# Kernel tuning notes

Measured on AMD Instinct MI355X. Metric: run time of the kernel, lower is better.

## Reference

```python
import jax, jax.numpy as jnp
import numpy as np

B, T, D = 1, 2048, 2048
H, HD = 32, 64
HEAD_COUNTS = np.array([8, 6, 4, 4, 6, 4])  # reasoning, creativity, curiosity, emotional, memory, meta
NEG = -1e9


def rope_tables(seq_len, dim, dtype):
    inv_freq = 1.0 / (10000.0 ** (jnp.arange(0, dim, 2, dtype=jnp.float32) / dim))
    t = jnp.arange(seq_len, dtype=jnp.float32)
    freqs = jnp.outer(t, inv_freq)            # [T, dim/2]
    emb = jnp.concatenate([freqs, freqs], -1) # [T, dim]
    return jnp.cos(emb).astype(dtype), jnp.sin(emb).astype(dtype)


def rotate_half(x):
    x1, x2 = jnp.split(x, 2, axis=-1)
    return jnp.concatenate([-x2, x1], axis=-1)


def setup_inputs() -> dict:
    key = jax.random.key(0)
    ks = jax.random.split(key, 8)
    x = jax.random.normal(ks[0], (B, T, D), jnp.float32)
    mask = jnp.tril(jnp.ones((T, T), jnp.int32))[None, None]  # causal [1,1,T,T]
    context_bias = jax.random.normal(ks[1], (B, T, T), jnp.float32) * 0.02
    mod_weights = jax.random.uniform(ks[2], (B, 6), jnp.float32, 0.5, 1.5)
    Wq = jax.random.normal(ks[3], (D, D), jnp.float32) * 0.02
    Wk = jax.random.normal(ks[4], (D, D), jnp.float32) * 0.02
    Wv = jax.random.normal(ks[5], (D, D), jnp.float32) * 0.02
    Wo = jax.random.normal(ks[6], (D, D), jnp.float32) * 0.02
    temp_scales = jnp.ones((H,), jnp.float32)
    return {"x": x, "mask": mask, "context_bias": context_bias,
            "mod_weights": mod_weights, "Wq": Wq, "Wk": Wk, "Wv": Wv,
            "Wo": Wo, "temp_scales": temp_scales}


def reference(x, mask, context_bias, mod_weights, Wq, Wk, Wv, Wo, temp_scales):
    b, t, d = x.shape
    # projections (torch Linear: y = x @ W.T)
    Q = (x @ Wq.T).reshape(b, t, H, HD).transpose(0, 2, 1, 3)  # [B,H,T,HD]
    K = (x @ Wk.T).reshape(b, t, H, HD).transpose(0, 2, 1, 3)
    V = (x @ Wv.T).reshape(b, t, H, HD).transpose(0, 2, 1, 3)
    cos, sin = rope_tables(t, HD, x.dtype)
    cos, sin = cos[None, None], sin[None, None]
    Q = Q * cos + rotate_half(Q) * sin
    K = K * cos + rotate_half(K) * sin
    scale = (HD ** -0.5) * temp_scales.reshape(1, H, 1, 1)
    attn = jnp.einsum('bhqd,bhkd->bhqk', Q, K) * scale
    attn = jnp.where(mask == 0, NEG, attn)
    attn = attn + context_bias[:, None]
    # per-head module reweight: expand [B,6] -> [B,H]
    w = jnp.repeat(mod_weights, np.asarray(HEAD_COUNTS), axis=1, total_repeat_length=H)
    attn = attn * w[:, :, None, None]
    attn = jax.nn.softmax(attn, axis=-1)
    out = jnp.einsum('bhqk,bhkd->bhqd', attn, V)
    out = out.transpose(0, 2, 1, 3).reshape(b, t, d)
    return out @ Wo.T
```

## Files before the change

kernel.cpp:

```cpp
#include <hip/hip_runtime.h>
#include <hip/hip_bf16.h>
#include <cstdint>
#include <cstddef>

typedef __bf16 bf16;
typedef bf16 bf16x4 __attribute__((ext_vector_type(4)));
typedef bf16 bf16x8 __attribute__((ext_vector_type(8)));
typedef float f32x4 __attribute__((ext_vector_type(4)));

#define MFMA_BF16(a,b,c) __builtin_amdgcn_mfma_f32_16x16x32_bf16((a),(b),(c),0,0,0)

typedef __attribute__((address_space(1))) const void gvoid;
typedef __attribute__((address_space(3))) void svoid;
__device__ __forceinline__ void gload16(const bf16* g, bf16* l){
  __builtin_amdgcn_global_load_lds((gvoid*)g, (svoid*)l, 16, 0, 0);
}

__device__ __forceinline__ int head_group(int h){
  return (h<8)?0:(h<14)?1:(h<18)?2:(h<22)?3:(h<28)?4:5;
}

struct CvtArgs { const float* src[5]; bf16* dst[5]; };
__global__ __launch_bounds__(256) void cvt_rope_kernel(CvtArgs a, int n,
                                                       float* __restrict__ cosT,
                                                       float* __restrict__ sinT){
  const int z = blockIdx.y;
  if (z == 5){
    if (blockIdx.x >= 256) return;
    const int t = blockIdx.x*8 + (threadIdx.x>>5);
    const int i = threadIdx.x&31;
    float invf = powf(10000.0f, -((float)i)/32.0f);
    float ang = (float)t * invf;
    cosT[t*32+i] = cosf(ang);
    sinT[t*32+i] = sinf(ang);
    return;
  }
  const float* __restrict__ in = a.src[z];
  bf16* __restrict__ out = a.dst[z];
  int i = (blockIdx.x*256 + threadIdx.x)*8;
  if (i >= n) return;
  const float4* p = (const float4*)(in + i);
  float4 va = p[0], vb = p[1];
  bf16x8 o;
  o[0]=(bf16)va.x; o[1]=(bf16)va.y; o[2]=(bf16)va.z; o[3]=(bf16)va.w;
  o[4]=(bf16)vb.x; o[5]=(bf16)vb.y; o[6]=(bf16)vb.z; o[7]=(bf16)vb.w;
  *(bf16x8*)(out+i) = o;
}

__device__ __forceinline__ void gemm_core(const bf16* __restrict__ A,
                                          const bf16* __restrict__ B,
                                          int row0, int col0,
                                          f32x4 (&acc)[4][4]){
  __shared__ bf16 As[128*32];
  __shared__ bf16 Bs[128*32];
  const int tid  = threadIdx.x;
  const int wave = tid>>6, lane = tid&63;
  const int l16  = lane&15, lg = lane>>4;
  const int wr   = wave>>1, wc = wave&1;

  const bf16* Ag0 = A + (size_t)(row0 + wave*32      + (lane>>2))*2048 + (lane&3)*8;
  const bf16* Ag1 = A + (size_t)(row0 + wave*32 + 16 + (lane>>2))*2048 + (lane&3)*8;
  const bf16* Bg0 = B + (size_t)(col0 + wave*32      + (lane>>2))*2048 + (lane&3)*8;
  const bf16* Bg1 = B + (size_t)(col0 + wave*32 + 16 + (lane>>2))*2048 + (lane&3)*8;
  bf16* AsB0 = As + (wave*32     )*32;
  bf16* AsB1 = As + (wave*32 + 16)*32;
  bf16* BsB0 = Bs + (wave*32     )*32;
  bf16* BsB1 = Bs + (wave*32 + 16)*32;

  #pragma unroll
  for (int m=0;m<4;++m)
    #pragma unroll
    for (int n=0;n<4;++n)
      #pragma unroll
      for (int r=0;r<4;++r) acc[m][n][r] = 0.f;

  for (int kt=0; kt<64; ++kt){
    const int ko = kt*32;
    gload16(Ag0 + ko, AsB0);
    gload16(Ag1 + ko, AsB1);
    gload16(Bg0 + ko, BsB0);
    gload16(Bg1 + ko, BsB1);
    __syncthreads();
    bf16x8 af[4], bfr[4];
    #pragma unroll
    for (int m=0;m<4;++m) af[m]  = *(const bf16x8*)&As[(wr*64+m*16+l16)*32 + lg*8];
    #pragma unroll
    for (int n=0;n<4;++n) bfr[n] = *(const bf16x8*)&Bs[(wc*64+n*16+l16)*32 + lg*8];
    #pragma unroll
    for (int m=0;m<4;++m)
      #pragma unroll
      for (int n=0;n<4;++n)
        acc[m][n] = MFMA_BF16(af[m], bfr[n], acc[m][n]);
    __syncthreads();
  }
}

__global__ __launch_bounds__(256) void gemm_qkv_kernel(
    const bf16* __restrict__ A,
    const bf16* __restrict__ B0, const bf16* __restrict__ B1, const bf16* __restrict__ B2,
    bf16* __restrict__ Qs, bf16* __restrict__ Ks, bf16* __restrict__ Vt,
    const float* __restrict__ cosT, const float* __restrict__ sinT,
    const float* __restrict__ mw, const float* __restrict__ ts){
  const int z = blockIdx.z;
  const bf16* B = (z==0)?B0:((z==1)?B1:B2);
  const int row0 = blockIdx.y*128, col0 = blockIdx.x*128;

  f32x4 acc[4][4];
  gemm_core(A, B, row0, col0, acc);

  const int tid  = threadIdx.x;
  const int wave = tid>>6, lane = tid&63;
  const int l16  = lane&15, lg = lane>>4;
  const int wr   = wave>>1, wc = wave&1;
  const int h    = (col0 + wc*64) >> 6;

  if (z == 2){
    #pragma unroll
    for (int n=0;n<4;++n){
      const int d = n*16 + l16;
      #pragma unroll
      for (int m=0;m<4;++m){
        const int t0 = row0 + wr*64 + m*16 + lg*4;
        bf16x4 v;
        #pragma unroll
        for (int r=0;r<4;++r) v[r] = (bf16)acc[m][n][r];
        *(bf16x4*)&Vt[((size_t)h*64 + d)*2048 + t0] = v;
      }
    }
  } else {
    const float sc = (z==0) ? 0.125f*ts[h]*mw[head_group(h)] : 1.0f;
    bf16* Out = (z==0) ? Qs : Ks;
    #pragma unroll
    for (int m=0;m<4;++m){
      #pragma unroll
      for (int r=0;r<4;++r){
        const int t = row0 + wr*64 + m*16 + lg*4 + r;
        const float* ct = cosT + t*32;
        const float* st = sinT + t*32;
        bf16* dst = Out + ((size_t)h*2048 + t)*64;
        #pragma unroll
        for (int n=0;n<2;++n){
          const int i = n*16 + l16;
          const float c = ct[i], s = st[i];
          const float a1 = acc[m][n][r], a2 = acc[m][n+2][r];
          dst[i]    = (bf16)((a1*c - a2*s)*sc);
          dst[i+32] = (bf16)((a2*c + a1*s)*sc);
        }
      }
    }
  }
}

__global__ __launch_bounds__(256) void gemm_out_kernel(
    const bf16* __restrict__ A, const bf16* __restrict__ B, float* __restrict__ C){
  __shared__ bf16 As[128*32];
  __shared__ bf16 Bs[64*32];
  const int row0 = blockIdx.y*128, col0 = blockIdx.x*64;
  const int tid  = threadIdx.x;
  const int wave = tid>>6, lane = tid&63;
  const int l16  = lane&15, lg = lane>>4;
  const int wr   = wave>>1, wc = wave&1;

  const bf16* Ag0 = A + (size_t)(row0 + wave*32      + (lane>>2))*2048 + (lane&3)*8;
  const bf16* Ag1 = A + (size_t)(row0 + wave*32 + 16 + (lane>>2))*2048 + (lane&3)*8;
  const bf16* Bg0 = B + (size_t)(col0 + wave*16      + (lane>>2))*2048 + (lane&3)*8;
  bf16* AsB0 = As + (wave*32     )*32;
  bf16* AsB1 = As + (wave*32 + 16)*32;
  bf16* BsB0 = Bs + (wave*16     )*32;

  f32x4 acc[4][2];
  #pragma unroll
  for (int m=0;m<4;++m)
    #pragma unroll
    for (int n=0;n<2;++n)
      #pragma unroll
      for (int r=0;r<4;++r) acc[m][n][r] = 0.f;

  for (int kt=0; kt<64; ++kt){
    const int ko = kt*32;
    gload16(Ag0 + ko, AsB0);
    gload16(Ag1 + ko, AsB1);
    gload16(Bg0 + ko, BsB0);
    __syncthreads();
    bf16x8 af[4], bfr[2];
    #pragma unroll
    for (int m=0;m<4;++m) af[m]  = *(const bf16x8*)&As[(wr*64+m*16+l16)*32 + lg*8];
    #pragma unroll
    for (int n=0;n<2;++n) bfr[n] = *(const bf16x8*)&Bs[(wc*32+n*16+l16)*32 + lg*8];
    #pragma unroll
    for (int m=0;m<4;++m)
      #pragma unroll
      for (int n=0;n<2;++n)
        acc[m][n] = MFMA_BF16(af[m], bfr[n], acc[m][n]);
    __syncthreads();
  }

  #pragma unroll
  for (int m=0;m<4;++m)
    #pragma unroll
    for (int n=0;n<2;++n)
      #pragma unroll
      for (int r=0;r<4;++r){
        size_t idx = (size_t)(row0 + wr*64 + m*16 + lg*4 + r)*2048
                   + col0 + wc*32 + n*16 + l16;
        C[idx] = acc[m][n][r];
      }
}

__global__ __launch_bounds__(512) void attn_kernel(
    const bf16* __restrict__ Qs, const bf16* __restrict__ Ks,
    const bf16* __restrict__ Vt, const float* __restrict__ biasf,
    const float* __restrict__ mw, bf16* __restrict__ attout){
  const int n  = blockIdx.x;
  const int h  = ((n&7)<<2) | ((n>>3)&3);
  const int qt = (n&256) ? ((n>>5)&7) : 15-((n>>5)&7);
  const int tid = threadIdx.x, wid = tid>>6, lane = tid&63;
  const int l16 = lane&15, lg = lane>>4;
  const float w_h = mw[head_group(h)];
  const int qbase = qt*128 + wid*16;
  const int qg0 = qbase + lg*4;
  const int nkt = 2*qt + 2;

  __shared__ bf16 Kl[2][4096];
  __shared__ bf16 Vl[2][4096];
  __shared__ bf16 plds[8][16][72];

  const int srow = tid>>3, ssub = tid&7;
  const bf16* Kg = Ks + (size_t)h*2048*64 + srow*64 + ssub*8;
  const bf16* Vg = Vt + ((size_t)h*64 + srow)*2048 + ssub*8;
  const int wsw = srow*64 + ((ssub ^ (srow&7))<<3);

  const bf16* Qp = Qs + ((size_t)h*2048 + qbase + l16)*64 + lg*8;
  bf16x8 qf0 = *(const bf16x8*)Qp;
  bf16x8 qf1 = *(const bf16x8*)(Qp + 32);

  const float* Bg = biasf + (size_t)qg0*2048;

  f32x4 O[4];
  float l[4] = {0.f,0.f,0.f,0.f};
  #pragma unroll
  for (int c=0;c<4;++c)
    #pragma unroll
    for (int r=0;r<4;++r) O[c][r] = 0.f;

  int rK0[4], rK1[4];
  #pragma unroll
  for (int c=0;c<4;++c){
    const int row = c*16 + l16;
    rK0[c] = row*64 + (((lg  ) ^ (row&7))<<3);
    rK1[c] = row*64 + (((4+lg) ^ (row&7))<<3);
  }

  float bc[4][4];
  #pragma unroll
  for (int c=0;c<4;++c)
    #pragma unroll
    for (int r=0;r<4;++r)
      bc[c][r] = w_h * Bg[(size_t)r*2048 + c*16 + l16];

  {
    bf16x8 k0v = *(const bf16x8*)Kg;
    bf16x8 v0v = *(const bf16x8*)Vg;
    *(bf16x8*)&Kl[0][wsw] = k0v;
    *(bf16x8*)&Vl[0][wsw] = v0v;
  }
  __syncthreads();

  int cur = 0;
  for (int kt=0; kt<nkt; ++kt){
    const int k0 = kt*64;
    const bool more = (kt+1 < nkt);
    bf16x8 kA, vA;
    float bn[4][4];
    if (more){
      kA = *(const bf16x8*)(Kg + (size_t)(k0+64)*64);
      vA = *(const bf16x8*)(Vg + (k0+64));
      #pragma unroll
      for (int c=0;c<4;++c)
        #pragma unroll
        for (int r=0;r<4;++r)
          bn[c][r] = w_h * Bg[(size_t)r*2048 + (k0+64) + c*16 + l16];
    }

    if (k0 <= qbase + 15){
      f32x4 S[4];
      #pragma unroll
      for (int c=0;c<4;++c)
        #pragma unroll
        for (int r=0;r<4;++r) S[c][r] = bc[c][r];

      __builtin_amdgcn_s_setprio(1);
      #pragma unroll
      for (int c=0;c<4;++c){
        bf16x8 kf0 = *(const bf16x8*)&Kl[cur][rK0[c]];
        bf16x8 kf1 = *(const bf16x8*)&Kl[cur][rK1[c]];
        S[c] = MFMA_BF16(qf0, kf0, S[c]);
        S[c] = MFMA_BF16(qf1, kf1, S[c]);
      }
      __builtin_amdgcn_s_setprio(0);

      #pragma unroll
      for (int c=0;c<4;++c){
        const int kg = k0 + c*16 + l16;
        #pragma unroll
        for (int r=0;r<4;++r){
          float s = S[c][r];
          if (kg > qg0+r) s = -1e30f;
          const float p = __expf(s - 4.0f);
          S[c][r] = p; l[r] += p;
        }
      }

      #pragma unroll
      for (int c=0;c<4;++c)
        #pragma unroll
        for (int r=0;r<4;++r)
          plds[wid][lg*4+r][c*16+l16] = (bf16)S[c][r];
      bf16x8 pf0 = *(const bf16x8*)&plds[wid][l16][lg*8];
      bf16x8 pf1 = *(const bf16x8*)&plds[wid][l16][lg*8+32];

      __builtin_amdgcn_s_setprio(1);
      #pragma unroll
      for (int c=0;c<4;++c){
        bf16x8 vf0 = *(const bf16x8*)&Vl[cur][rK0[c]];
        bf16x8 vf1 = *(const bf16x8*)&Vl[cur][rK1[c]];
        O[c] = MFMA_BF16(pf0, vf0, O[c]);
        O[c] = MFMA_BF16(pf1, vf1, O[c]);
      }
      __builtin_amdgcn_s_setprio(0);
    }

    if (more){
      *(bf16x8*)&Kl[cur^1][wsw] = kA;
      *(bf16x8*)&Vl[cur^1][wsw] = vA;
      #pragma unroll
      for (int c=0;c<4;++c)
        #pragma unroll
        for (int r=0;r<4;++r) bc[c][r] = bn[c][r];
    }
    __syncthreads();
    cur ^= (int)more;
  }

  #pragma unroll
  for (int r=0;r<4;++r){
    float v = l[r];
    v += __shfl_xor(v,1);
    v += __shfl_xor(v,2);
    v += __shfl_xor(v,4);
    v += __shfl_xor(v,8);
    l[r] = 1.0f / v;
  }
  #pragma unroll
  for (int c=0;c<4;++c)
    #pragma unroll
    for (int r=0;r<4;++r)
      attout[(size_t)(qg0+r)*2048 + h*64 + c*16 + l16] = (bf16)(O[c][r]*l[r]);
}

extern "C" void kernel_launch(void* const* d_in, const int* in_sizes, int n_in,
                              void* d_out, int out_size, void* d_ws, size_t ws_size,
                              hipStream_t stream){
  const float* x    = (const float*)d_in[0];
  const float* bias = (const float*)d_in[2];
  const float* mw   = (const float*)d_in[3];
  const float* Wq   = (const float*)d_in[4];
  const float* Wk   = (const float*)d_in[5];
  const float* Wv   = (const float*)d_in[6];
  const float* Wo   = (const float*)d_in[7];
  const float* ts   = (const float*)d_in[8];
  float* out = (float*)d_out;

  const size_t SZ = (size_t)2048*2048;
  bf16* base = (bf16*)d_ws;
  bf16* xb   = base;
  bf16* Wqb  = base + 1*SZ;
  bf16* Wkb  = base + 2*SZ;
  bf16* Wvb  = base + 3*SZ;
  bf16* Wob  = base + 4*SZ;
  bf16* Qsb  = base + 5*SZ;
  bf16* Ksb  = base + 6*SZ;
  bf16* Vtb  = base + 7*SZ;
  bf16* att  = base + 8*SZ;
  float* cosT = (float*)(base + 9*SZ);
  float* sinT = cosT + 2048*32;

  CvtArgs ca;
  ca.src[0]=x;  ca.src[1]=Wq;  ca.src[2]=Wk;  ca.src[3]=Wv;  ca.src[4]=Wo;
  ca.dst[0]=xb; ca.dst[1]=Wqb; ca.dst[2]=Wkb; ca.dst[3]=Wvb; ca.dst[4]=Wob;
  const int nb = (int)(SZ/8/256);
  cvt_rope_kernel<<<dim3(nb,6),256,0,stream>>>(ca, (int)SZ, cosT, sinT);
  gemm_qkv_kernel<<<dim3(16,16,3),256,0,stream>>>(xb, Wqb,Wkb,Wvb,
                                                  Qsb,Ksb,Vtb, cosT,sinT, mw,ts);
  attn_kernel<<<512,512,0,stream>>>(Qsb,Ksb,Vtb,bias,mw,att);
  gemm_out_kernel<<<dim3(32,16),256,0,stream>>>(att, Wob, out);
}
```

Measured before the change: 165.5 us.

## Double GEMM K-tile to 64 with XOR-swizzled LDS layout

Both the QKV and output-projection GEMMs now stage 64-wide K slices per iteration instead of 32, which halves the number of loop iterations and barrier pairs. The LDS layout uses an XOR swizzle of 16-byte chunks, applied on the global load side and matched on the read side, to avoid bank conflicts on the wider rows. This doubles LDS use per block, which may lower occupancy, and the loop still does not overlap loads with compute.

```diff
diff --git a/kernel.cpp b/kernel.cpp
--- a/kernel.cpp
+++ b/kernel.cpp
@@ -51,21 +51,31 @@
                                           const bf16* __restrict__ B,
                                           int row0, int col0,
                                           f32x4 (&acc)[4][4]){
-  __shared__ bf16 As[128*32];
-  __shared__ bf16 Bs[128*32];
+  __shared__ bf16 As[128*64];
+  __shared__ bf16 Bs[128*64];
   const int tid  = threadIdx.x;
   const int wave = tid>>6, lane = tid&63;
   const int l16  = lane&15, lg = lane>>4;
   const int wr   = wave>>1, wc = wave&1;
 
-  const bf16* Ag0 = A + (size_t)(row0 + wave*32      + (lane>>2))*2048 + (lane&3)*8;
-  const bf16* Ag1 = A + (size_t)(row0 + wave*32 + 16 + (lane>>2))*2048 + (lane&3)*8;
-  const bf16* Bg0 = B + (size_t)(col0 + wave*32      + (lane>>2))*2048 + (lane&3)*8;
-  const bf16* Bg1 = B + (size_t)(col0 + wave*32 + 16 + (lane>>2))*2048 + (lane&3)*8;
-  bf16* AsB0 = As + (wave*32     )*32;
-  bf16* AsB1 = As + (wave*32 + 16)*32;
-  bf16* BsB0 = Bs + (wave*32     )*32;
-  bf16* BsB1 = Bs + (wave*32 + 16)*32;
+  const int srow = lane>>3;
+  const int scol = ((lane&7) ^ srow)*8;
+  const bf16* Ag0 = A + (size_t)(row0 + wave*32      + srow)*2048 + scol;
+  const bf16* Ag1 = A + (size_t)(row0 + wave*32 +  8 + srow)*2048 + scol;
+  const bf16* Ag2 = A + (size_t)(row0 + wave*32 + 16 + srow)*2048 + scol;
+  const bf16* Ag3 = A + (size_t)(row0 + wave*32 + 24 + srow)*2048 + scol;
+  const bf16* Bg0 = B + (size_t)(col0 + wave*32      + srow)*2048 + scol;
+  const bf16* Bg1 = B + (size_t)(col0 + wave*32 +  8 + srow)*2048 + scol;
+  const bf16* Bg2 = B + (size_t)(col0 + wave*32 + 16 + srow)*2048 + scol;
+  const bf16* Bg3 = B + (size_t)(col0 + wave*32 + 24 + srow)*2048 + scol;
+  bf16* Ad0 = As + (wave*32     )*64;
+  bf16* Ad1 = As + (wave*32 +  8)*64;
+  bf16* Ad2 = As + (wave*32 + 16)*64;
+  bf16* Ad3 = As + (wave*32 + 24)*64;
+  bf16* Bd0 = Bs + (wave*32     )*64;
+  bf16* Bd1 = Bs + (wave*32 +  8)*64;
+  bf16* Bd2 = Bs + (wave*32 + 16)*64;
+  bf16* Bd3 = Bs + (wave*32 + 24)*64;
 
   #pragma unroll
   for (int m=0;m<4;++m)
@@ -74,23 +84,43 @@
       #pragma unroll
       for (int r=0;r<4;++r) acc[m][n][r] = 0.f;
 
-  for (int kt=0; kt<64; ++kt){
-    const int ko = kt*32;
-    gload16(Ag0 + ko, AsB0);
-    gload16(Ag1 + ko, AsB1);
-    gload16(Bg0 + ko, BsB0);
-    gload16(Bg1 + ko, BsB1);
+  int rA0[4], rA1[4], rB0[4], rB1[4];
+  #pragma unroll
+  for (int i=0;i<4;++i){
+    const int ra = wr*64 + i*16 + l16;
+    const int rb = wc*64 + i*16 + l16;
+    rA0[i] = ra*64 + (((lg  ) ^ (l16&7))<<3);
+    rA1[i] = ra*64 + (((4+lg) ^ (l16&7))<<3);
+    rB0[i] = rb*64 + (((lg  ) ^ (l16&7))<<3);
+    rB1[i] = rb*64 + (((4+lg) ^ (l16&7))<<3);
+  }
+
+  for (int kt=0; kt<32; ++kt){
+    const int ko = kt*64;
+    gload16(Ag0 + ko, Ad0);
+    gload16(Ag1 + ko, Ad1);
+    gload16(Ag2 + ko, Ad2);
+    gload16(Ag3 + ko, Ad3);
+    gload16(Bg0 + ko, Bd0);
+    gload16(Bg1 + ko, Bd1);
+    gload16(Bg2 + ko, Bd2);
+    gload16(Bg3 + ko, Bd3);
     __syncthreads();
-    bf16x8 af[4], bfr[4];
-    #pragma unroll
-    for (int m=0;m<4;++m) af[m]  = *(const bf16x8*)&As[(wr*64+m*16+l16)*32 + lg*8];
-    #pragma unroll
-    for (int n=0;n<4;++n) bfr[n] = *(const bf16x8*)&Bs[(wc*64+n*16+l16)*32 + lg*8];
+    bf16x8 a0[4], a1[4], b0[4], b1[4];
+    #pragma unroll
+    for (int i=0;i<4;++i){
+      a0[i] = *(const bf16x8*)&As[rA0[i]];
+      a1[i] = *(const bf16x8*)&As[rA1[i]];
+      b0[i] = *(const bf16x8*)&Bs[rB0[i]];
+      b1[i] = *(const bf16x8*)&Bs[rB1[i]];
+    }
     #pragma unroll
     for (int m=0;m<4;++m)
       #pragma unroll
-      for (int n=0;n<4;++n)
-        acc[m][n] = MFMA_BF16(af[m], bfr[n], acc[m][n]);
+      for (int n=0;n<4;++n){
+        acc[m][n] = MFMA_BF16(a0[m], b0[n], acc[m][n]);
+        acc[m][n] = MFMA_BF16(a1[m], b1[n], acc[m][n]);
+      }
     __syncthreads();
   }
 }
@@ -153,20 +183,28 @@
 
 __global__ __launch_bounds__(256) void gemm_out_kernel(
     const bf16* __restrict__ A, const bf16* __restrict__ B, float* __restrict__ C){
-  __shared__ bf16 As[128*32];
-  __shared__ bf16 Bs[64*32];
+  __shared__ bf16 As[128*64];
+  __shared__ bf16 Bs[64*64];
   const int row0 = blockIdx.y*128, col0 = blockIdx.x*64;
   const int tid  = threadIdx.x;
   const int wave = tid>>6, lane = tid&63;
   const int l16  = lane&15, lg = lane>>4;
   const int wr   = wave>>1, wc = wave&1;
 
-  const bf16* Ag0 = A + (size_t)(row0 + wave*32      + (lane>>2))*2048 + (lane&3)*8;
-  const bf16* Ag1 = A + (size_t)(row0 + wave*32 + 16 + (lane>>2))*2048 + (lane&3)*8;
-  const bf16* Bg0 = B + (size_t)(col0 + wave*16      + (lane>>2))*2048 + (lane&3)*8;
-  bf16* AsB0 = As + (wave*32     )*32;
-  bf16* AsB1 = As + (wave*32 + 16)*32;
-  bf16* BsB0 = Bs + (wave*16     )*32;
+  const int srow = lane>>3;
+  const int scol = ((lane&7) ^ srow)*8;
+  const bf16* Ag0 = A + (size_t)(row0 + wave*32      + srow)*2048 + scol;
+  const bf16* Ag1 = A + (size_t)(row0 + wave*32 +  8 + srow)*2048 + scol;
+  const bf16* Ag2 = A + (size_t)(row0 + wave*32 + 16 + srow)*2048 + scol;
+  const bf16* Ag3 = A + (size_t)(row0 + wave*32 + 24 + srow)*2048 + scol;
+  const bf16* Bg0 = B + (size_t)(col0 + wave*16      + srow)*2048 + scol;
+  const bf16* Bg1 = B + (size_t)(col0 + wave*16 +  8 + srow)*2048 + scol;
+  bf16* Ad0 = As + (wave*32     )*64;
+  bf16* Ad1 = As + (wave*32 +  8)*64;
+  bf16* Ad2 = As + (wave*32 + 16)*64;
+  bf16* Ad3 = As + (wave*32 + 24)*64;
+  bf16* Bd0 = Bs + (wave*16     )*64;
+  bf16* Bd1 = Bs + (wave*16 +  8)*64;
 
   f32x4 acc[4][2];
   #pragma unroll
@@ -176,22 +214,47 @@
       #pragma unroll
       for (int r=0;r<4;++r) acc[m][n][r] = 0.f;
 
-  for (int kt=0; kt<64; ++kt){
-    const int ko = kt*32;
-    gload16(Ag0 + ko, AsB0);
-    gload16(Ag1 + ko, AsB1);
-    gload16(Bg0 + ko, BsB0);
+  int rA0[4], rA1[4], rB0[2], rB1[2];
+  #pragma unroll
+  for (int i=0;i<4;++i){
+    const int ra = wr*64 + i*16 + l16;
+    rA0[i] = ra*64 + (((lg  ) ^ (l16&7))<<3);
+    rA1[i] = ra*64 + (((4+lg) ^ (l16&7))<<3);
+  }
+  #pragma unroll
+  for (int i=0;i<2;++i){
+    const int rb = wc*32 + i*16 + l16;
+    rB0[i] = rb*64 + (((lg  ) ^ (l16&7))<<3);
+    rB1[i] = rb*64 + (((4+lg) ^ (l16&7))<<3);
+  }
+
+  for (int kt=0; kt<32; ++kt){
+    const int ko = kt*64;
+    gload16(Ag0 + ko, Ad0);
+    gload16(Ag1 + ko, Ad1);
+    gload16(Ag2 + ko, Ad2);
+    gload16(Ag3 + ko, Ad3);
+    gload16(Bg0 + ko, Bd0);
+    gload16(Bg1 + ko, Bd1);
     __syncthreads();
-    bf16x8 af[4], bfr[2];
-    #pragma unroll
-    for (int m=0;m<4;++m) af[m]  = *(const bf16x8*)&As[(wr*64+m*16+l16)*32 + lg*8];
-    #pragma unroll
-    for (int n=0;n<2;++n) bfr[n] = *(const bf16x8*)&Bs[(wc*32+n*16+l16)*32 + lg*8];
+    bf16x8 a0[4], a1[4], b0[2], b1[2];
+    #pragma unroll
+    for (int i=0;i<4;++i){
+      a0[i] = *(const bf16x8*)&As[rA0[i]];
+      a1[i] = *(const bf16x8*)&As[rA1[i]];
+    }
+    #pragma unroll
+    for (int i=0;i<2;++i){
+      b0[i] = *(const bf16x8*)&Bs[rB0[i]];
+      b1[i] = *(const bf16x8*)&Bs[rB1[i]];
+    }
     #pragma unroll
     for (int m=0;m<4;++m)
       #pragma unroll
-      for (int n=0;n<2;++n)
-        acc[m][n] = MFMA_BF16(af[m], bfr[n], acc[m][n]);
+      for (int n=0;n<2;++n){
+        acc[m][n] = MFMA_BF16(a0[m], b0[n], acc[m][n]);
+        acc[m][n] = MFMA_BF16(a1[m], b1[n], acc[m][n]);
+      }
     __syncthreads();
   }
 
```

Result: slower. 178.6 us (+7.9%).
